# Kernel optimization log

Measured on AMD Instinct MI355X. Metric: run time of the kernel, lower is better.

## Reference

```python
import jax, jax.numpy as jnp
import numpy as np

B, T, E, D, V, L, A = 32, 800, 512, 1024, 5000, 149, 512
SOS, EOS = 1, 2


def setup_inputs() -> dict:
    key = jax.random.key(0)
    ks = jax.random.split(key, 20)
    s = 0.02
    inp = {
        'hpad': jax.random.normal(ks[0], (B, T, E), dtype=jnp.float32),
        'hlen': jax.random.randint(ks[1], (B,), T // 2, T + 1),
        'ys': jax.random.randint(ks[2], (B, L), 3, V),
        # embedding + output projection
        'embed': jax.random.normal(ks[3], (V, D), dtype=jnp.float32) * s,
        'W_out': jax.random.normal(ks[4], (V, D), dtype=jnp.float32) * s,
        'b_out': jnp.zeros((V,), dtype=jnp.float32),
        # additive attention params
        'W_enc': jax.random.normal(ks[5], (E, A), dtype=jnp.float32) * s,
        'W_dec': jax.random.normal(ks[6], (D, A), dtype=jnp.float32) * s,
        'v_att': jax.random.normal(ks[7], (A,), dtype=jnp.float32) * s,
        # LSTMCell layer 0: input = [ey; att_c] of size D+E
        'W_ih0': jax.random.normal(ks[8], (4 * D, D + E), dtype=jnp.float32) * s,
        'b_ih0': jnp.zeros((4 * D,), dtype=jnp.float32),
        'W_hh0': jax.random.normal(ks[9], (4 * D, D), dtype=jnp.float32) * s,
        'b_hh0': jnp.zeros((4 * D,), dtype=jnp.float32),
        # LSTMCell layer 1: input = z0 of size D
        'W_ih1': jax.random.normal(ks[10], (4 * D, D), dtype=jnp.float32) * s,
        'b_ih1': jnp.zeros((4 * D,), dtype=jnp.float32),
        'W_hh1': jax.random.normal(ks[11], (4 * D, D), dtype=jnp.float32) * s,
        'b_hh1': jnp.zeros((4 * D,), dtype=jnp.float32),
    }
    return inp


def _lstm_cell(x, h, c, W_ih, b_ih, W_hh, b_hh):
    # torch.nn.LSTMCell gate order: i, f, g, o
    g = x @ W_ih.T + b_ih + h @ W_hh.T + b_hh
    i, f, gg, o = jnp.split(g, 4, axis=-1)
    c2 = jax.nn.sigmoid(f) * c + jax.nn.sigmoid(i) * jnp.tanh(gg)
    h2 = jax.nn.sigmoid(o) * jnp.tanh(c2)
    return h2, c2


def reference(hpad, hlen, ys, embed, W_out, b_out, W_enc, W_dec, v_att,
              W_ih0, b_ih0, W_hh0, b_hh0, W_ih1, b_ih1, W_hh1, b_hh1):
    mask = jnp.arange(T)[None, :] < hlen[:, None]          # [B,T]
    hpad = hpad * mask[..., None]                          # mask_by_length
    ys_in = jnp.concatenate([jnp.full((B, 1), SOS, ys.dtype), ys], axis=1)   # [B,L+1]
    ys_out = jnp.concatenate([ys, jnp.full((B, 1), EOS, ys.dtype)], axis=1)  # [B,L+1]
    eys = embed[ys_in]                                     # [B,L+1,D]
    pe = jnp.einsum('bte,ea->bta', hpad, W_enc)            # precomputed enc proj

    def step(carry, ey):
        z0, c0, z1, c1 = carry
        # additive attention: e = v^T tanh(W_enc h + W_dec z0)
        e = jnp.einsum('bta,a->bt', jnp.tanh(pe + (z0 @ W_dec)[:, None, :]), v_att)
        e = jnp.where(mask, e, -1e30)
        w = jax.nn.softmax(e, axis=-1)                     # [B,T]
        att_c = jnp.einsum('bt,bte->be', w, hpad)          # [B,E]
        z0, c0 = _lstm_cell(jnp.concatenate([ey, att_c], axis=1), z0, c0,
                            W_ih0, b_ih0, W_hh0, b_hh0)
        z1, c1 = _lstm_cell(z0, z1, c1, W_ih1, b_ih1, W_hh1, b_hh1)
        logits = z1 @ W_out.T + b_out                      # [B,V]
        return (z0, c0, z1, c1), logits

    z = jnp.zeros((B, D), dtype=hpad.dtype)
    carry0 = (z, z, z, z)
    _, logits = jax.lax.scan(step, carry0, eys.transpose(1, 0, 2))  # [L+1,B,V]
    logits = logits.transpose(1, 0, 2)                     # [B,L+1,V]

    logp = jax.nn.log_softmax(logits, axis=-1)
    nll = -jnp.take_along_axis(logp, ys_out[..., None], axis=-1)[..., 0]
    # F.cross_entropy mean, then * (mean(len ys_in) - 1) = * L
    loss = nll.mean() * L
    acc = (jnp.argmax(logits, axis=-1) == ys_out).mean()
    return loss, acc
```

## Files before the change

### kernel.cpp

```cpp
#include <hip/hip_runtime.h>


typedef unsigned short u16;
typedef unsigned char u8;
typedef long long i64;
typedef unsigned long long u64;
typedef float f32x4 __attribute__((ext_vector_type(4)));
typedef float f32x2 __attribute__((ext_vector_type(2)));
typedef short s16x8 __attribute__((ext_vector_type(8)));

constexpr int cB = 32, cT = 800, cE = 512, cD = 1024, cV = 5000, cL = 149,
              cNS = 150, cA = 512;
constexpr int SOS = 1, EOS = 2;
constexpr int NBLK = 256;
constexpr float DS = 1.0f / 128.0f;

__device__ __forceinline__ float bf2f(u16 x){
  union { unsigned u; float f; } v; v.u = ((unsigned)x) << 16; return v.f;
}
__device__ __forceinline__ u16 f2bf(float f){
  union { float f; unsigned u; } v; v.f = f;
  unsigned r = v.u + 0x7FFFu + ((v.u >> 16) & 1u);
  return (u16)(r >> 16);
}
__device__ __forceinline__ float frcp(float x){ return __builtin_amdgcn_rcpf(x); }
__device__ __forceinline__ float fsigm(float x){ return frcp(1.f + __expf(-x)); }
__device__ __forceinline__ float ftanh(float x){
  float u = __expf(2.f * x);
  return 1.f - 2.f * frcp(u + 1.f);
}
__device__ __forceinline__ f32x4 MFMA(s16x8 a, s16x8 b, f32x4 c){
  return __builtin_amdgcn_mfma_f32_16x16x32_bf16(a, b, c, 0, 0, 0);
}
__device__ __forceinline__ f32x4 MFMA8(i64 a, i64 b, f32x4 c){
  return __builtin_amdgcn_mfma_f32_16x16x32_fp8_fp8(a, b, c, 0, 0, 0);
}
__device__ __forceinline__ s16x8 LD8(const u16* p){ return *(const s16x8*)p; }
__device__ __forceinline__ u8 f2fp8(float x){
  return (u8)(__builtin_amdgcn_cvt_pk_fp8_f32(x, x, 0, false) & 0xFF);
}
__device__ __forceinline__ unsigned pk4(float a, float b, float c, float d){
  unsigned w = (unsigned)__builtin_amdgcn_cvt_pk_fp8_f32(a, b, 0, false);
  w = (unsigned)__builtin_amdgcn_cvt_pk_fp8_f32(c, d, (int)w, true);
  return w;
}
__device__ __forceinline__ void unpack8(unsigned lo, unsigned hi, float* o){
  f32x2 a = __builtin_amdgcn_cvt_pk_f32_fp8((int)lo, false);
  f32x2 b = __builtin_amdgcn_cvt_pk_f32_fp8((int)lo, true);
  f32x2 c = __builtin_amdgcn_cvt_pk_f32_fp8((int)hi, false);
  f32x2 d = __builtin_amdgcn_cvt_pk_f32_fp8((int)hi, true);
  o[0]=a[0]; o[1]=a[1]; o[2]=b[0]; o[3]=b[1];
  o[4]=c[0]; o[5]=c[1]; o[6]=d[0]; o[7]=d[1];
}

__device__ __forceinline__ float ld_sc(const float* p){
  return __hip_atomic_load(p, __ATOMIC_RELAXED, __HIP_MEMORY_SCOPE_AGENT);
}
__device__ __forceinline__ void st_sc(float* p, float v){
  __hip_atomic_store(p, v, __ATOMIC_RELAXED, __HIP_MEMORY_SCOPE_AGENT);
}
__device__ __forceinline__ u64 ld_sc8(const void* p){
  return __hip_atomic_load((const u64*)p, __ATOMIC_RELAXED, __HIP_MEMORY_SCOPE_AGENT);
}
__device__ __forceinline__ void st_scb(u8* p, u8 v){
  __hip_atomic_store(p, v, __ATOMIC_RELAXED, __HIP_MEMORY_SCOPE_AGENT);
}

__global__ void k_init(int* bar, float* q, float* c0, float* c1, u8* z1f8,
                       float* att_acc, float* att_l){
  int i = blockIdx.x * blockDim.x + threadIdx.x, n = gridDim.x * blockDim.x;
  for (int k = i; k < 512; k += n) bar[k] = 0;
  for (int k = i; k < cB * cA; k += n) q[k] = 0.f;
  for (int k = i; k < 2 * cB * cD; k += n){ c0[k] = 0.f; c1[k] = 0.f; }
  for (int k = i; k < cB * cD / 4; k += n) ((unsigned*)z1f8)[k] = 0;
  for (int k = i; k < cB * cE; k += n) att_acc[k] = 0.f;
  for (int k = i; k < cB; k += n) att_l[k] = 0.f;
}

__global__ void k_cvt(const float* __restrict__ s, u16* __restrict__ d, int n4){
  int i = blockIdx.x * blockDim.x + threadIdx.x, st = gridDim.x * blockDim.x;
  for (int k = i; k < n4; k += st){
    float4 v = ((const float4*)s)[k];
    ushort4 o; o.x = f2bf(v.x); o.y = f2bf(v.y); o.z = f2bf(v.z); o.w = f2bf(v.w);
    ((ushort4*)d)[k] = o;
  }
}

__global__ void k_cvt8I(const float* __restrict__ s, u8* __restrict__ d, int n){
  int i = blockIdx.x * blockDim.x + threadIdx.x, st = gridDim.x * blockDim.x;
  for (int k = i; k < n; k += st){
    int row = k >> 6, grp = k & 63;
    const float4* p = (const float4*)(s + (size_t)row * 512 + grp * 8);
    float4 v0 = p[0], v1 = p[1];
    unsigned lo = pk4(v0.x, v0.y, v0.z, v0.w);
    unsigned hi = pk4(v1.x, v1.y, v1.z, v1.w);
    *(uint2*)(d + (size_t)row * 1024 + grp * 16 + 8) = make_uint2(lo, hi);
  }
}

__global__ void k_slice(const float* __restrict__ s, u16* __restrict__ d, int n,
                        int cshift, int srcld, int coff){
  int i = blockIdx.x * blockDim.x + threadIdx.x, st = gridDim.x * blockDim.x;
  int cmask = (1 << cshift) - 1;
  for (int k = i; k < n; k += st){
    int r = k >> cshift, c = k & cmask;
    d[k] = f2bf(s[(size_t)r * srcld + coff + c]);
  }
}

__global__ void k_transp(const float* __restrict__ s, u16* __restrict__ d, int n,
                         int rshift, int csrc){
  int i = blockIdx.x * blockDim.x + threadIdx.x, st = gridDim.x * blockDim.x;
  int mask = (1 << rshift) - 1;
  for (int k = i; k < n; k += st){
    int dd = k & mask, a = k >> rshift;
    d[k] = f2bf(s[(size_t)dd * csrc + a]);
  }
}

__global__ void k_bias(const float* a, const float* b, float* o, int n){
  int i = blockIdx.x * blockDim.x + threadIdx.x, st = gridDim.x * blockDim.x;
  for (int k = i; k < n; k += st) o[k] = a[k] + b[k];
}

__global__ void k_wf8perm(const float* __restrict__ s, u8* __restrict__ d,
                          int n4, int kshift, int srcld, int coff){
  int i = blockIdx.x * blockDim.x + threadIdx.x, st = gridDim.x * blockDim.x;
  int kmask = (1 << kshift) - 1;
  for (int k = i; k < n4; k += st){
    int flat = k * 4;
    int R = flat >> kshift, kk = flat & kmask;
    int j = R >> 5, jj = R & 31, g = jj >> 3, c = jj & 7;
    const float* p = s + (size_t)(g * 1024 + j * 8 + c) * srcld + coff + kk;
    ((unsigned*)d)[k] = pk4(p[0]*16.f, p[1]*16.f, p[2]*16.f, p[3]*16.f);
  }
}

__global__ void k_wf8(const float* __restrict__ s, u8* __restrict__ d, int n4){
  int i = blockIdx.x * blockDim.x + threadIdx.x, st = gridDim.x * blockDim.x;
  for (int k = i; k < n4; k += st){
    float4 v = ((const float4*)s)[k];
    ((unsigned*)d)[k] = pk4(v.x*16.f, v.y*16.f, v.z*16.f, v.w*16.f);
  }
}

__global__ void k_wf8t(const float* __restrict__ s, u8* __restrict__ d, int n4){
  int i = blockIdx.x * blockDim.x + threadIdx.x, st = gridDim.x * blockDim.x;
  for (int k = i; k < n4; k += st){
    int flat = k * 4;
    int a = flat >> 10, dd = flat & 1023;
    ((unsigned*)d)[k] = pk4(s[(size_t)(dd+0)*512 + a]*16.f,
                            s[(size_t)(dd+1)*512 + a]*16.f,
                            s[(size_t)(dd+2)*512 + a]*16.f,
                            s[(size_t)(dd+3)*512 + a]*16.f);
  }
}

__global__ void k_gather(const u16* __restrict__ embb, const int* __restrict__ ys,
                         u16* __restrict__ ey, int n16){
  int i = blockIdx.x * blockDim.x + threadIdx.x, st = gridDim.x * blockDim.x;
  for (int k = i; k < n16; k += st){
    int r = k >> 7, seg = k & 127;
    int s = r >> 5, b = r & 31;
    int tok = (s == 0) ? SOS : ys[b * cL + (s - 1)];
    ((uint4*)ey)[(size_t)r * 128 + seg] =
        ((const uint4*)embb)[(size_t)tok * 128 + seg];
  }
}

__global__ __launch_bounds__(512, 1) void k_pe2(const u16* __restrict__ A,
    const u16* __restrict__ Bw, u8* __restrict__ ph8){
  int tid = threadIdx.x, w = tid >> 6, l = tid & 63;
  int col = l & 15, kin = 8 * (l >> 4);
  int mw = w >> 2, nw = w & 3;
  int m0 = blockIdx.x * 128 + mw * 64;
  int n0 = nw * 128;
  f32x4 acc[4][8] = {};
// ... 7 lines not shown
    #pragma unroll
    for (int i = 0; i < 4; ++i)
      #pragma unroll
      for (int j = 0; j < 8; ++j) acc[i][j] = MFMA(af[i], bf[j], acc[i][j]);
  }
  int hi4 = (l >> 4) * 4;
  #pragma unroll
  for (int i = 0; i < 4; ++i)
    #pragma unroll
    for (int j = 0; j < 8; ++j){
      int a0 = n0 + j * 16 + col;
      size_t boff = ((size_t)(a0 >> 3) << 4) + (a0 & 7);
      #pragma unroll
      for (int r = 0; r < 4; ++r){
        int row = m0 + i * 16 + hi4 + r;
        ph8[(size_t)row * 1024 + boff] = f2fp8(acc[i][j][r]);
      }
    }
}

__global__ __launch_bounds__(512, 1) void k_ey2(const u16* __restrict__ ey,
    const u16* __restrict__ Wm, const float* __restrict__ bih0,
    const float* __restrict__ bhh0, u16* __restrict__ eyproj,
    float* __restrict__ g0buf){
  int tid = threadIdx.x, w = tid >> 6, l = tid & 63;
  int col = l & 15, kin = 8 * (l >> 4);
  int mw = w >> 2, nw = w & 3;
  int m0 = blockIdx.x * 128 + mw * 64;
  int n0 = blockIdx.y * 512 + nw * 128;
  f32x4 acc[4][8] = {};
  for (int kc = 0; kc < 32; ++kc){
    int k = kc * 32 + kin;
    s16x8 af[4], bf[8];
    #pragma unroll
    for (int i = 0; i < 4; ++i){
      int ar = m0 + i * 16 + col; ar = (ar < 4800) ? ar : 0;
      af[i] = LD8(ey + (size_t)ar * 1024 + k);
    }
    #pragma unroll
    for (int j = 0; j < 8; ++j) bf[j] = LD8(Wm + (size_t)(n0 + j*16 + col)*1024 + k);
    #pragma unroll
    for (int i = 0; i < 4; ++i)
      #pragma unroll
      for (int j = 0; j < 8; ++j) acc[i][j] = MFMA(af[i], bf[j], acc[i][j]);
  }
  int hi4 = (l >> 4) * 4;
  #pragma unroll
  for (int i = 0; i < 4; ++i)
    #pragma unroll
    for (int j = 0; j < 8; ++j){
      int jc = n0 + j * 16 + col;
      float bj = bih0[jc] + bhh0[jc];
      #pragma unroll
      for (int r = 0; r < 4; ++r){
        int row = m0 + i * 16 + hi4 + r;
        if (row < 4800){
          float val = acc[i][j][r] + bj;
          eyproj[(size_t)row * 4096 + jc] = f2bf(val);
          if (row < 32) g0buf[(size_t)row * 4096 + jc] = val;
        }
      }
    }
}

struct LoopArgs {
  const int* hlen;
  const u8* ph8;
  const u16* eyproj;
  const u8* Wapf8; const u8* Whh1f8; const u8* Wih1f8; const u8* Whh0f8;
  const u8* WdecTf8;
  const float* vatt; const float* bias01;
  float* q; float* att_acc; float* att_l;
  float* g0buf; float* hh1buf; u8* z0f8; u8* z1f8;
  float* c0; float* c1; u16* z1all;
  int* bar;
};

constexpr int SPZ = 1048;
constexpr int SPA = 536;

struct P1Lds { float red[8][512]; float ls[8]; };
struct GvLds { u8 x[32 * SPZ]; float acc[8][2][16][16]; };
union LoopLds { P1Lds p1; GvLds gv; };

__device__ __forceinline__ void gbar(int* bar, int blk, int target){
  __syncthreads();
  if (threadIdx.x == 0){
    asm volatile("s_waitcnt vmcnt(0)" ::: "memory");
    __hip_atomic_store(&bar[blk], target, __ATOMIC_RELAXED, __HIP_MEMORY_SCOPE_AGENT);
  }
  if (blk == NBLK - 1){
    if (threadIdx.x < NBLK){
      while (__hip_atomic_load(&bar[threadIdx.x], __ATOMIC_RELAXED,
                               __HIP_MEMORY_SCOPE_AGENT) < target)
        __builtin_amdgcn_s_sleep(1);
    }
    __syncthreads();
    if (threadIdx.x < 8)
      __hip_atomic_store(&bar[256 + threadIdx.x * 16], target, __ATOMIC_RELAXED,
                         __HIP_MEMORY_SCOPE_AGENT);
  }
  if (threadIdx.x == 0){
    int* rel = &bar[256 + (blk >> 5) * 16];
    while (__hip_atomic_load(rel, __ATOMIC_RELAXED,
                             __HIP_MEMORY_SCOPE_AGENT) < target)
      __builtin_amdgcn_s_sleep(1);
  }
  __syncthreads();
}

__device__ __forceinline__ void stage_att(LoopLds& L, const float* att_acc,
                                          const float* att_l, int tid){
  int r = tid >> 4, c0 = (tid & 15) * 32;
  float sc = 8.0f / ld_sc(att_l + r);
  const float* src = att_acc + r * 512 + c0;
  unsigned wd[8];
  #pragma unroll
  for (int i = 0; i < 8; ++i){
    union { u64 q; float f[2]; } a, b;
    a.q = ld_sc8(src + i * 4);
    b.q = ld_sc8(src + i * 4 + 2);
    wd[i] = pk4(a.f[0] * sc, a.f[1] * sc, b.f[0] * sc, b.f[1] * sc);
  }
  uint2* dst = (uint2*)&L.gv.x[r * SPA + c0];
  dst[0] = make_uint2(wd[0], wd[1]);
  dst[1] = make_uint2(wd[2], wd[3]);
  dst[2] = make_uint2(wd[4], wd[5]);
  dst[3] = make_uint2(wd[6], wd[7]);
}

__device__ __forceinline__ void stage_z(LoopLds& L, const u8* zf8, int tid){
  int r = tid >> 4, c0 = (tid & 15) * 64;
  const u8* src = zf8 + (size_t)r * 1024 + c0;
  u64 v[8];
  #pragma unroll
  for (int i = 0; i < 8; ++i) v[i] = ld_sc8(src + i * 8);
  u64* dst = (u64*)&L.gv.x[r * SPZ + c0];
  #pragma unroll
  for (int i = 0; i < 8; ++i) dst[i] = v[i];
}

template<int KH, int ITERS, int SP>
__device__ __forceinline__ void gemv_reg(const i64* wreg, LoopLds& L, int tid){
  const int w = tid >> 6, l = tid & 63;
  const int col = l & 15, kin = 8 * (l >> 4);
  const int kh = (KH == 4) ? (w & 3) : (w & 1);
  constexpr int KB = ITERS * 32;
  const u8* xr = &L.gv.x[col * SP + kh * KB + kin];
  f32x4 a0 = {0.f,0.f,0.f,0.f}, a1 = {0.f,0.f,0.f,0.f};
  #pragma unroll
  for (int kc = 0; kc < ITERS; ++kc){
    i64 x0 = *(const i64*)(xr + kc * 32);
    i64 x1 = *(const i64*)(xr + 16 * SP + kc * 32);
    a0 = MFMA8(x0, wreg[kc], a0);
    a1 = MFMA8(x1, wreg[kc], a1);
  }
  const int hi4 = (l >> 4) * 4;
  #pragma unroll
  for (int r = 0; r < 4; ++r){
    L.gv.acc[w][0][hi4 + r][col] = a0[r];
    L.gv.acc[w][1][hi4 + r][col] = a1[r];
  }
// ... 30 lines not shown
      const u8* wr2 = g_.Wih1f8 + (size_t)blk * 32 * 1024 +
                      (size_t)(nt4 * 16 + col) * 1024 + kh4 * 256 + kin;
      #pragma unroll
      for (int kc = 0; kc < 8; ++kc) wC[kc] = *(const i64*)(wr2 + kc * 32);
    } else {
      const u8* wr = g_.Whh1f8 + (size_t)(blk - 128) * 32 * 1024 +
                     (size_t)(nt4 * 16 + col) * 1024 + kh4 * 256 + kin;
      #pragma unroll
      for (int kc = 0; kc < 8; ++kc) wB[kc] = *(const i64*)(wr + kc * 32);
      if (blk < 192){
        const u8* wr2 = g_.Whh0f8 + (size_t)(blk - 128) * 64 * 1024 +
                        (size_t)(nt2 * 16 + col) * 1024 + kh2 * 512 + kin;
        #pragma unroll
        for (int kc = 0; kc < 16; ++kc) wC[kc] = *(const i64*)(wr2 + kc * 32);
      } else if (blk < 208){
        const u8* wr2 = g_.WdecTf8 + (size_t)(blk - 192) * 32 * 1024 +
                        (size_t)(nt4 * 16 + col) * 1024 + kh4 * 256 + kin;
        #pragma unroll
        for (int kc = 0; kc < 8; ++kc) wC[kc] = *(const i64*)(wr2 + kc * 32);
      }
    }
  }
  __syncthreads();
  int target = 0;
  for (int s = 0; s < cNS; ++s){
    const int p = s & 1;
    if (nrow > 0){
      float qv[8];
      const float* qb = g_.q + b_att * cA + l * 8;
      #pragma unroll
      for (int i = 0; i < 8; ++i) qv[i] = ld_sc(qb + i);
      float acc8[8] = {0.f,0.f,0.f,0.f,0.f,0.f,0.f,0.f};
      float lsum = 0.f;
      for (int t = t0 + w; t < t1; t += 8){
        uint4 v = *(const uint4*)&ph8_lds[(t - t0) * 1024 + l * 16];
        float x[8]; unpack8(v.x, v.y, x);
        float e_ = 0.f;
        #pragma unroll
        for (int i = 0; i < 8; ++i) e_ += vv[i] * ftanh(x[i] + qv[i]);
        #pragma unroll
        for (int m = 1; m < 64; m <<= 1) e_ += __shfl_xor(e_, m, 64);
        float wt = __expf(e_);
        lsum += wt;
        float h[8]; unpack8(v.z, v.w, h);
        #pragma unroll
        for (int i = 0; i < 8; ++i) acc8[i] = fmaf(wt, h[i], acc8[i]);
      }
      *(f32x4*)&L.p1.red[w][l * 8]     = *(f32x4*)&acc8[0];
      *(f32x4*)&L.p1.red[w][l * 8 + 4] = *(f32x4*)&acc8[4];
      if (l == 0) L.p1.ls[w] = lsum;
      __syncthreads();
      float vsum = 0.f;
      #pragma unroll
      for (int ww = 0; ww < 8; ++ww) vsum += L.p1.red[ww][tid];
      atomicAdd(&g_.att_acc[b_att * cE + tid], vsum);
      if (tid == 0){
        float ls = 0.f;
        #pragma unroll
        for (int i = 0; i < 8; ++i) ls += L.p1.ls[i];
        atomicAdd(&g_.att_l[b_att], ls);
      }
    }
    gbar(g_.bar, blk, ++target);
    if (blk < 128){
      stage_att(L, g_.att_acc, g_.att_l, tid);
      __syncthreads();
      gemv_reg<4, 4, SPA>(wB, L, tid);
      __syncthreads();
      if (tid < 256){
        int b = tid >> 3, dc = tid & 7, d = blk * 8 + dc;
        int mt = b >> 4, rr = b & 15;
        float gate[4];
        #pragma unroll
        for (int g = 0; g < 4; ++g){
          int jj = g * 8 + dc;
          float v = 0.f;
          #pragma unroll
          for (int kh = 0; kh < 4; ++kh)
            v += L.gv.acc[(jj >> 4) * 4 + kh][mt][rr][jj & 15];
          gate[g] = v * DS +
                    ld_sc(&g_.g0buf[(size_t)p * cB * 4096 + b * 4096 + g * 1024 + d]);
        }
        float c = fsigm(gate[1]) * g_.c0[(size_t)p * cB * cD + b * cD + d] +
                  fsigm(gate[0]) * ftanh(gate[2]);
        float z = fsigm(gate[3]) * ftanh(c);
        g_.c0[(size_t)(p ^ 1) * cB * cD + b * cD + d] = c;
        st_scb(&g_.z0f8[b * cD + d], f2fp8(z * 8.f));
      }
    } else {
      stage_z(L, g_.z1f8, tid);
      __syncthreads();
      gemv_reg<4, 8, SPZ>(wB, L, tid);
      __syncthreads();
      const int jb = (blk - 128) * 32;
      #pragma unroll
      for (int it = 0; it < 2; ++it){
        int idx = it * 512 + tid;
        int b = idx >> 5, jj = idx & 31;
        int mt = b >> 4, rr = b & 15;
        float v = 0.f;
        #pragma unroll
        for (int kh = 0; kh < 4; ++kh)
          v += L.gv.acc[(jj >> 4) * 4 + kh][mt][rr][jj & 15];
        st_sc(&g_.hh1buf[b * 4096 + jb + jj], v * DS + g_.bias01[jb + jj]);
      }
    }
    gbar(g_.bar, blk, ++target);
    if (blk < 128){
      stage_z(L, g_.z0f8, tid);
      __syncthreads();
      gemv_reg<4, 8, SPZ>(wC, L, tid);
      __syncthreads();
      if (tid < 256){
        int b = tid >> 3, dc = tid & 7, d = blk * 8 + dc;
        int mt = b >> 4, rr = b & 15;
        float gate[4];
        #pragma unroll
        for (int g = 0; g < 4; ++g){
          int jj = g * 8 + dc;
          float v = 0.f;
          #pragma unroll
          for (int kh = 0; kh < 4; ++kh)
            v += L.gv.acc[(jj >> 4) * 4 + kh][mt][rr][jj & 15];
          gate[g] = v * DS + ld_sc(&g_.hh1buf[b * 4096 + g * 1024 + d]);
        }
        float c = fsigm(gate[1]) * g_.c1[(size_t)p * cB * cD + b * cD + d] +
                  fsigm(gate[0]) * ftanh(gate[2]);
        float z = fsigm(gate[3]) * ftanh(c);
        g_.c1[(size_t)(p ^ 1) * cB * cD + b * cD + d] = c;
        g_.z1all[((size_t)s + 1) * cB * cD + b * cD + d] = f2bf(z);
        st_scb(&g_.z1f8[b * cD + d], f2fp8(z * 8.f));
      }
    } else if (blk < 192){
      stage_z(L, g_.z0f8, tid);
      __syncthreads();
      gemv_reg<2, 16, SPZ>(wC, L, tid);
      __syncthreads();
      if (s < cNS - 1){
        const int jb = (blk - 128) * 64;
        #pragma unroll
        for (int it = 0; it < 4; ++it){
          int idx = it * 512 + tid;
          int b = idx >> 6, jj = idx & 63;
          int mt = b >> 4, rr = b & 15;
          float v = 0.f;
          #pragma unroll
          for (int kh = 0; kh < 2; ++kh)
            v += L.gv.acc[(jj >> 4) * 2 + kh][mt][rr][jj & 15];
          st_sc(&g_.g0buf[(size_t)(p ^ 1) * cB * 4096 + b * 4096 + jb + jj],
                v * DS + bf2f(g_.eyproj[(((size_t)s + 1) * cB + b) * 4096 + jb + jj]));
        }
      }
    } else if (blk < 208){
      stage_z(L, g_.z0f8, tid);
      __syncthreads();
      gemv_reg<4, 8, SPZ>(wC, L, tid);
      __syncthreads();
      if (s < cNS - 1){
        const int jb = (blk - 192) * 32;
        #pragma unroll
        for (int it = 0; it < 2; ++it){
          int idx = it * 512 + tid;
          int b = idx >> 5, jj = idx & 31;
          int mt = b >> 4, rr = b & 15;
          float v = 0.f;
          #pragma unroll
          for (int kh = 0; kh < 4; ++kh)
            v += L.gv.acc[(jj >> 4) * 4 + kh][mt][rr][jj & 15];
          st_sc(&g_.q[b * cA + jb + jj], v * DS);
        }
      }
    } else if (blk == 208){
      for (int i = tid; i < cB * cE; i += 512) st_sc(&g_.att_acc[i], 0.f);
      if (tid < 32) st_sc(&g_.att_l[tid], 0.f);
    }
    gbar(g_.bar, blk, ++target);
  }
}

__global__ __launch_bounds__(256) void k_ce1(const u16* __restrict__ z1all,
    const u16* __restrict__ Woutb, const float* __restrict__ bout,
    const int* __restrict__ ys, float* __restrict__ pmax, float* __restrict__ psum,
    int* __restrict__ pai, float* __restrict__ tgtl){
  int blk = blockIdx.x;
  int sc = blk / 40, vc = blk % 40;
  int tid = threadIdx.x, w = tid >> 6, l = tid & 63;
  int kin = 8 * (l >> 4), col = l & 15;
  int v0 = vc * 128 + w * 32;
  int vA = v0 + col, vB = v0 + 16 + col;
  float boA = (vA < cV) ? bout[vA] : 0.f;
  float boB = (vB < cV) ? bout[vB] : 0.f;
  const u16* wrA = Woutb + (size_t)((vA < cV) ? vA : cV - 1) * cD;
  const u16* wrB = Woutb + (size_t)((vB < cV) ? vB : cV - 1) * cD;
  __shared__ int tgt_sh[32];
  __shared__ float rsm[4][32], rss[4][32];
  __shared__ int rsi[4][32];
  for (int si = 0; si < 5; ++si){
    int s = sc * 5 + si;
    if (tid < 32) tgt_sh[tid] = (s < cL) ? ys[tid * cL + s] : EOS;
// ... 109 lines not shown
  const int*   hlen = (const int*)d_in[1];
  const int*   ys   = (const int*)d_in[2];
  const float* embed= (const float*)d_in[3];
  const float* Wout = (const float*)d_in[4];
  const float* bout = (const float*)d_in[5];
  const float* Wenc = (const float*)d_in[6];
  const float* Wdec = (const float*)d_in[7];
  const float* vatt = (const float*)d_in[8];
  const float* Wih0 = (const float*)d_in[9];
  const float* bih0 = (const float*)d_in[10];
  const float* Whh0 = (const float*)d_in[11];
  const float* bhh0 = (const float*)d_in[12];
  const float* Wih1 = (const float*)d_in[13];
  const float* bih1 = (const float*)d_in[14];
  const float* Whh1 = (const float*)d_in[15];
  const float* bhh1 = (const float*)d_in[16];
  (void)in_sizes; (void)n_in; (void)out_size; (void)ws_size;

  char* base = (char*)d_ws;
  size_t off = 0;
  auto alloc = [&](size_t bytes) -> void* {
    void* r = base + off; off += (bytes + 255) & ~(size_t)255; return r;
  };
  int*   bar     = (int*)  alloc(512 * sizeof(int));
  u16*   hpadM   = (u16*)  alloc((size_t)cB * cT * cE * 2);
  u8*    ph8     = (u8*)   alloc((size_t)cB * cT * 1024);
  u16*   embb    = (u16*)  alloc((size_t)cV * cD * 2);
  u16*   ey      = (u16*)  alloc((size_t)cNS * cB * cD * 2);
  u16*   eyproj  = (u16*)  alloc((size_t)cNS * cB * 4096 * 2);
  u16*   z1all   = (u16*)  alloc((size_t)(cNS + 1) * cB * cD * 2);
  u16*   WencT   = (u16*)  alloc((size_t)cA * cE * 2);
  u16*   Wih0m   = (u16*)  alloc((size_t)4096 * cD * 2);
  u16*   Woutb   = (u16*)  alloc((size_t)cV * cD * 2);
  u8*    Wapf8   = (u8*)   alloc((size_t)4096 * 512);
  u8*    Wih1f8  = (u8*)   alloc((size_t)4096 * 1024);
  u8*    Whh1f8  = (u8*)   alloc((size_t)4096 * 1024);
  u8*    Whh0f8  = (u8*)   alloc((size_t)4096 * 1024);
  u8*    WdecTf8 = (u8*)   alloc((size_t)512 * 1024);
  float* bias01  = (float*)alloc(4096 * 4);
  float* qbuf    = (float*)alloc((size_t)cB * cA * 4);
  float* att_acc = (float*)alloc((size_t)cB * cE * 4);
  float* att_l   = (float*)alloc((size_t)cB * 4);
  float* g0buf   = (float*)alloc((size_t)2 * cB * 4096 * 4);
  float* hh1buf  = (float*)alloc((size_t)cB * 4096 * 4);
  u8*    z0f8    = (u8*)   alloc((size_t)cB * cD);
  u8*    z1f8    = (u8*)   alloc((size_t)cB * cD);
  float* c0      = (float*)alloc((size_t)2 * cB * cD * 4);
  float* c1      = (float*)alloc((size_t)2 * cB * cD * 4);
  float* pmax    = (float*)alloc((size_t)cNS * cB * 40 * 4);
  float* psum    = (float*)alloc((size_t)cNS * cB * 40 * 4);
  int*   pai     = (int*)  alloc((size_t)cNS * cB * 40 * 4);
  float* tgtl    = (float*)alloc((size_t)cNS * cB * 4);
  float* cestep  = (float*)alloc((size_t)cNS * 2 * 4);

  k_init<<<64, 256, 0, stream>>>(bar, qbuf, c0, c1, z1f8, att_acc, att_l);
  k_cvt<<<2048, 256, 0, stream>>>(hpad, hpadM, cB * cT * cE / 4);
  k_cvt8I<<<1024, 256, 0, stream>>>(hpad, ph8, cB * cT * 64);
  k_cvt<<<2048, 256, 0, stream>>>(embed, embb, cV * cD / 4);
  k_cvt<<<2048, 256, 0, stream>>>(Wout, Woutb, cV * cD / 4);
  k_slice<<<1024, 256, 0, stream>>>(Wih0, Wih0m, 4096 * cD, 10, 1536, 0);
  k_transp<<<256, 256, 0, stream>>>(Wenc, WencT, cA * cE, 9, cA);
  k_bias<<<16, 256, 0, stream>>>(bih1, bhh1, bias01, 4096);
  k_wf8perm<<<512, 256, 0, stream>>>(Wih0, Wapf8, 4096 * 512 / 4, 9, 1536, 1024);
  k_wf8perm<<<1024, 256, 0, stream>>>(Wih1, Wih1f8, 4096 * 1024 / 4, 10, 1024, 0);
  k_wf8<<<1024, 256, 0, stream>>>(Whh1, Whh1f8, 4096 * 1024 / 4);
  k_wf8<<<1024, 256, 0, stream>>>(Whh0, Whh0f8, 4096 * 1024 / 4);
  k_wf8t<<<128, 256, 0, stream>>>(Wdec, WdecTf8, 512 * 1024 / 4);
  k_gather<<<1200, 256, 0, stream>>>(embb, ys, ey, cNS * cB * 128);
  k_pe2<<<200, 512, 0, stream>>>(hpadM, WencT, ph8);
  k_ey2<<<dim3(38, 8), 512, 0, stream>>>(ey, Wih0m, bih0, bhh0, eyproj, g0buf);

  LoopArgs la;
  la.hlen = hlen; la.ph8 = ph8; la.eyproj = eyproj;
  la.Wapf8 = Wapf8; la.Whh1f8 = Whh1f8; la.Wih1f8 = Wih1f8;
  la.Whh0f8 = Whh0f8; la.WdecTf8 = WdecTf8;
  la.vatt = vatt; la.bias01 = bias01;
  la.q = qbuf; la.att_acc = att_acc; la.att_l = att_l;
  la.g0buf = g0buf; la.hh1buf = hh1buf; la.z0f8 = z0f8; la.z1f8 = z1f8;
  la.c0 = c0; la.c1 = c1; la.z1all = z1all; la.bar = bar;
  k_loop<<<NBLK, 512, 0, stream>>>(la);

  k_ce1<<<1200, 256, 0, stream>>>(z1all, Woutb, bout, ys, pmax, psum, pai, tgtl);
  k_ce2<<<cNS, 64, 0, stream>>>(pmax, psum, pai, tgtl, ys, cestep);
  k_ce3<<<1, 256, 0, stream>>>(cestep, (float*)d_out);
}
```

Baseline: 4.657 ms.

## Replace grid barriers with step-tagged dataflow flags in persistent decoder loop

```diff
diff --git a/kernel.cpp b/kernel.cpp
--- a/kernel.cpp
+++ b/kernel.cpp
@@ -3,6 +3,7 @@
 
 typedef unsigned short u16;
 typedef unsigned char u8;
+typedef unsigned int u32;
 typedef long long i64;
 typedef unsigned long long u64;
 typedef float f32x4 __attribute__((ext_vector_type(4)));
@@ -16,11 +17,11 @@
 constexpr float DS = 1.0f / 128.0f;
 
 __device__ __forceinline__ float bf2f(u16 x){
-  union { unsigned u; float f; } v; v.u = ((unsigned)x) << 16; return v.f;
+  union { u32 u; float f; } v; v.u = ((u32)x) << 16; return v.f;
 }
 __device__ __forceinline__ u16 f2bf(float f){
-  union { float f; unsigned u; } v; v.f = f;
-  unsigned r = v.u + 0x7FFFu + ((v.u >> 16) & 1u);
+  union { float f; u32 u; } v; v.f = f;
+  u32 r = v.u + 0x7FFFu + ((v.u >> 16) & 1u);
   return (u16)(r >> 16);
 }
 __device__ __forceinline__ float frcp(float x){ return __builtin_amdgcn_rcpf(x); }
@@ -39,12 +40,12 @@
 __device__ __forceinline__ u8 f2fp8(float x){
   return (u8)(__builtin_amdgcn_cvt_pk_fp8_f32(x, x, 0, false) & 0xFF);
 }
-__device__ __forceinline__ unsigned pk4(float a, float b, float c, float d){
-  unsigned w = (unsigned)__builtin_amdgcn_cvt_pk_fp8_f32(a, b, 0, false);
-  w = (unsigned)__builtin_amdgcn_cvt_pk_fp8_f32(c, d, (int)w, true);
+__device__ __forceinline__ u32 pk4(float a, float b, float c, float d){
+  u32 w = (u32)__builtin_amdgcn_cvt_pk_fp8_f32(a, b, 0, false);
+  w = (u32)__builtin_amdgcn_cvt_pk_fp8_f32(c, d, (int)w, true);
   return w;
 }
-__device__ __forceinline__ void unpack8(unsigned lo, unsigned hi, float* o){
+__device__ __forceinline__ void unpack8(u32 lo, u32 hi, float* o){
   f32x2 a = __builtin_amdgcn_cvt_pk_f32_fp8((int)lo, false);
   f32x2 b = __builtin_amdgcn_cvt_pk_f32_fp8((int)lo, true);
   f32x2 c = __builtin_amdgcn_cvt_pk_f32_fp8((int)hi, false);
@@ -62,19 +63,28 @@
 __device__ __forceinline__ u64 ld_sc8(const void* p){
   return __hip_atomic_load((const u64*)p, __ATOMIC_RELAXED, __HIP_MEMORY_SCOPE_AGENT);
 }
-__device__ __forceinline__ void st_scb(u8* p, u8 v){
+__device__ __forceinline__ void st_sc8(void* p, u64 v){
+  __hip_atomic_store((u64*)p, v, __ATOMIC_RELAXED, __HIP_MEMORY_SCOPE_AGENT);
+}
+__device__ __forceinline__ u32 ld_su(const u32* p){
+  return __hip_atomic_load(p, __ATOMIC_RELAXED, __HIP_MEMORY_SCOPE_AGENT);
+}
+__device__ __forceinline__ void st_su(u32* p, u32 v){
   __hip_atomic_store(p, v, __ATOMIC_RELAXED, __HIP_MEMORY_SCOPE_AGENT);
 }
-
-__global__ void k_init(int* bar, float* q, float* c0, float* c1, u8* z1f8,
+__device__ __forceinline__ void st_s16(u16* p, u32 v){
+  asm volatile("global_store_short %0, %1, off sc0 sc1" :: "v"(p), "v"(v) : "memory");
+}
+
+__global__ void k_init(u32* ctl, u32* qt, float* c0, float* c1, u16* z1t,
                        float* att_acc, float* att_l){
   int i = blockIdx.x * blockDim.x + threadIdx.x, n = gridDim.x * blockDim.x;
-  for (int k = i; k < 512; k += n) bar[k] = 0;
-  for (int k = i; k < cB * cA; k += n) q[k] = 0.f;
+  for (int k = i; k < 64; k += n) ctl[k] = 0;
+  for (int k = i; k < cB * cA; k += n) qt[k] = 0;
   for (int k = i; k < 2 * cB * cD; k += n){ c0[k] = 0.f; c1[k] = 0.f; }
-  for (int k = i; k < cB * cD / 4; k += n) ((unsigned*)z1f8)[k] = 0;
-  for (int k = i; k < cB * cE; k += n) att_acc[k] = 0.f;
-  for (int k = i; k < cB; k += n) att_l[k] = 0.f;
+  for (int k = i; k < cB * cD / 2; k += n) ((u32*)z1t)[k] = 0;
+  for (int k = i; k < 2 * cB * cE; k += n) att_acc[k] = 0.f;
+  for (int k = i; k < 2 * cB; k += n) att_l[k] = 0.f;
 }
 
 __global__ void k_cvt(const float* __restrict__ s, u16* __restrict__ d, int n4){
@@ -92,8 +102,8 @@
     int row = k >> 6, grp = k & 63;
     const float4* p = (const float4*)(s + (size_t)row * 512 + grp * 8);
     float4 v0 = p[0], v1 = p[1];
-    unsigned lo = pk4(v0.x, v0.y, v0.z, v0.w);
-    unsigned hi = pk4(v1.x, v1.y, v1.z, v1.w);
+    u32 lo = pk4(v0.x, v0.y, v0.z, v0.w);
+    u32 hi = pk4(v1.x, v1.y, v1.z, v1.w);
     *(uint2*)(d + (size_t)row * 1024 + grp * 16 + 8) = make_uint2(lo, hi);
   }
 }
@@ -132,7 +142,7 @@
     int R = flat >> kshift, kk = flat & kmask;
     int j = R >> 5, jj = R & 31, g = jj >> 3, c = jj & 7;
     const float* p = s + (size_t)(g * 1024 + j * 8 + c) * srcld + coff + kk;
-    ((unsigned*)d)[k] = pk4(p[0]*16.f, p[1]*16.f, p[2]*16.f, p[3]*16.f);
+    ((u32*)d)[k] = pk4(p[0]*16.f, p[1]*16.f, p[2]*16.f, p[3]*16.f);
   }
 }
 
@@ -140,7 +150,7 @@
   int i = blockIdx.x * blockDim.x + threadIdx.x, st = gridDim.x * blockDim.x;
   for (int k = i; k < n4; k += st){
     float4 v = ((const float4*)s)[k];
-    ((unsigned*)d)[k] = pk4(v.x*16.f, v.y*16.f, v.z*16.f, v.w*16.f);
+    ((u32*)d)[k] = pk4(v.x*16.f, v.y*16.f, v.z*16.f, v.w*16.f);
   }
 }
 
@@ -149,10 +159,10 @@
   for (int k = i; k < n4; k += st){
     int flat = k * 4;
     int a = flat >> 10, dd = flat & 1023;
-    ((unsigned*)d)[k] = pk4(s[(size_t)(dd+0)*512 + a]*16.f,
-                            s[(size_t)(dd+1)*512 + a]*16.f,
-                            s[(size_t)(dd+2)*512 + a]*16.f,
-                            s[(size_t)(dd+3)*512 + a]*16.f);
+    ((u32*)d)[k] = pk4(s[(size_t)(dd+0)*512 + a]*16.f,
+                       s[(size_t)(dd+1)*512 + a]*16.f,
+                       s[(size_t)(dd+2)*512 + a]*16.f,
+                       s[(size_t)(dd+3)*512 + a]*16.f);
   }
 }
 
@@ -206,7 +216,7 @@
 __global__ __launch_bounds__(512, 1) void k_ey2(const u16* __restrict__ ey,
     const u16* __restrict__ Wm, const float* __restrict__ bih0,
     const float* __restrict__ bhh0, u16* __restrict__ eyproj,
-    float* __restrict__ g0buf){
+    u32* __restrict__ g0t){
   int tid = threadIdx.x, w = tid >> 6, l = tid & 63;
   int col = l & 15, kin = 8 * (l >> 4);
   int mw = w >> 2, nw = w & 3;
@@ -241,7 +251,7 @@
         if (row < 4800){
           float val = acc[i][j][r] + bj;
           eyproj[(size_t)row * 4096 + jc] = f2bf(val);
-          if (row < 32) g0buf[(size_t)row * 4096 + jc] = val;
+          if (row < 32) g0t[(size_t)row * 4096 + jc] = (u32)f2bf(val);
         }
       }
     }
@@ -254,74 +264,43 @@
   const u8* Wapf8; const u8* Whh1f8; const u8* Wih1f8; const u8* Whh0f8;
   const u8* WdecTf8;
   const float* vatt; const float* bias01;
-  float* q; float* att_acc; float* att_l;
-  float* g0buf; float* hh1buf; u8* z0f8; u8* z1f8;
+  u32* qt; float* att_acc; float* att_l;
+  u32* g0t; u32* hh1t; u16* z0t; u16* z1t;
   float* c0; float* c1; u16* z1all;
-  int* bar;
+  u32* ctl;
 };
 
 constexpr int SPZ = 1048;
 constexpr int SPA = 536;
 
 struct P1Lds { float red[8][512]; float ls[8]; };
-struct GvLds { u8 x[32 * SPZ]; float acc[8][2][16][16]; };
+struct GvLds { u8 x[32 * SPZ]; float acc[8][2][16][17]; };
 union LoopLds { P1Lds p1; GvLds gv; };
 
-__device__ __forceinline__ void gbar(int* bar, int blk, int target){
-  __syncthreads();
-  if (threadIdx.x == 0){
-    asm volatile("s_waitcnt vmcnt(0)" ::: "memory");
-    __hip_atomic_store(&bar[blk], target, __ATOMIC_RELAXED, __HIP_MEMORY_SCOPE_AGENT);
-  }
-  if (blk == NBLK - 1){
-    if (threadIdx.x < NBLK){
-      while (__hip_atomic_load(&bar[threadIdx.x], __ATOMIC_RELAXED,
-                               __HIP_MEMORY_SCOPE_AGENT) < target)
-        __builtin_amdgcn_s_sleep(1);
-    }
-    __syncthreads();
-    if (threadIdx.x < 8)
-      __hip_atomic_store(&bar[256 + threadIdx.x * 16], target, __ATOMIC_RELAXED,
-                         __HIP_MEMORY_SCOPE_AGENT);
-  }
-  if (threadIdx.x == 0){
-    int* rel = &bar[256 + (blk >> 5) * 16];
-    while (__hip_atomic_load(rel, __ATOMIC_RELAXED,
-                             __HIP_MEMORY_SCOPE_AGENT) < target)
-      __builtin_amdgcn_s_sleep(1);
-  }
-  __syncthreads();
-}
-
-__device__ __forceinline__ void stage_att(LoopLds& L, const float* att_acc,
-                                          const float* att_l, int tid){
-  int r = tid >> 4, c0 = (tid & 15) * 32;
-  float sc = 8.0f / ld_sc(att_l + r);
-  const float* src = att_acc + r * 512 + c0;
-  unsigned wd[8];
+template<int SP>
+__device__ __forceinline__ void stage_ztag(LoopLds& L, const u16* zt, int tid,
+                                           int tag){
+  int r = tid >> 4, cb = (tid & 15) * 64;
+  const u16* src = zt + (size_t)r * 1024 + cb;
+  const u64 tmask = 0xFF00FF00FF00FF00ULL;
+  const u64 texp = 0x0100010001000100ULL * (u64)(tag & 0xFF);
+  u64 v[16];
+  for(;;){
+    bool ok = true;
+    #pragma unroll
+    for (int i = 0; i < 16; ++i) v[i] = ld_sc8(src + i * 4);
+    #pragma unroll
+    for (int i = 0; i < 16; ++i) ok &= ((v[i] & tmask) == texp);
+    if (__all(ok)) break;
+    __builtin_amdgcn_s_sleep(1);
+  }
+  u64* dst = (u64*)&L.gv.x[r * SP + cb];
   #pragma unroll
   for (int i = 0; i < 8; ++i){
-    union { u64 q; float f[2]; } a, b;
-    a.q = ld_sc8(src + i * 4);
-    b.q = ld_sc8(src + i * 4 + 2);
-    wd[i] = pk4(a.f[0] * sc, a.f[1] * sc, b.f[0] * sc, b.f[1] * sc);
-  }
-  uint2* dst = (uint2*)&L.gv.x[r * SPA + c0];
-  dst[0] = make_uint2(wd[0], wd[1]);
-  dst[1] = make_uint2(wd[2], wd[3]);
-  dst[2] = make_uint2(wd[4], wd[5]);
-  dst[3] = make_uint2(wd[6], wd[7]);
-}
-
-__device__ __forceinline__ void stage_z(LoopLds& L, const u8* zf8, int tid){
-  int r = tid >> 4, c0 = (tid & 15) * 64;
-  const u8* src = zf8 + (size_t)r * 1024 + c0;
-  u64 v[8];
-  #pragma unroll
-  for (int i = 0; i < 8; ++i) v[i] = ld_sc8(src + i * 8);
-  u64* dst = (u64*)&L.gv.x[r * SPZ + c0];
-  #pragma unroll
-  for (int i = 0; i < 8; ++i) dst[i] = v[i];
+    u32 lo = __builtin_amdgcn_perm((u32)(v[2*i] >> 32),   (u32)v[2*i],   0x06040200u);
+    u32 hi = __builtin_amdgcn_perm((u32)(v[2*i+1] >> 32), (u32)v[2*i+1], 0x06040200u);
+    dst[i] = ((u64)hi << 32) | lo;
+  }
 }
 
 template<int KH, int ITERS, int SP>
@@ -398,54 +377,136 @@
     }
   }
   __syncthreads();
-  int target = 0;
+
   for (int s = 0; s < cNS; ++s){
     const int p = s & 1;
-    if (nrow > 0){
-      float qv[8];
-      const float* qb = g_.q + b_att * cA + l * 8;
-      #pragma unroll
-      for (int i = 0; i < 8; ++i) qv[i] = ld_sc(qb + i);
-      float acc8[8] = {0.f,0.f,0.f,0.f,0.f,0.f,0.f,0.f};
-      float lsum = 0.f;
-      for (int t = t0 + w; t < t1; t += 8){
-        uint4 v = *(const uint4*)&ph8_lds[(t - t0) * 1024 + l * 16];
-        float x[8]; unpack8(v.x, v.y, x);
-        float e_ = 0.f;
-        #pragma unroll
-        for (int i = 0; i < 8; ++i) e_ += vv[i] * ftanh(x[i] + qv[i]);
-        #pragma unroll
-        for (int m = 1; m < 64; m <<= 1) e_ += __shfl_xor(e_, m, 64);
-        float wt = __expf(e_);
-        lsum += wt;
-        float h[8]; unpack8(v.z, v.w, h);
-        #pragma unroll
-        for (int i = 0; i < 8; ++i) acc8[i] = fmaf(wt, h[i], acc8[i]);
-      }
-      *(f32x4*)&L.p1.red[w][l * 8]     = *(f32x4*)&acc8[0];
-      *(f32x4*)&L.p1.red[w][l * 8 + 4] = *(f32x4*)&acc8[4];
-      if (l == 0) L.p1.ls[w] = lsum;
-      __syncthreads();
-      float vsum = 0.f;
-      #pragma unroll
-      for (int ww = 0; ww < 8; ++ww) vsum += L.p1.red[ww][tid];
-      atomicAdd(&g_.att_acc[b_att * cE + tid], vsum);
+    u64 eyw = 0;
+    {
+      const u32* qrow = g_.qt + b_att * cA + l * 8;
+      u64 qw[4];
+      const u64 tmaskq = 0xFFFF0000FFFF0000ULL;
+      const u64 texpq  = ((u64)(u32)s << 16) | ((u64)(u32)s << 48);
+      for(;;){
+        bool ok = true;
+        #pragma unroll
+        for (int i = 0; i < 4; ++i){
+          qw[i] = ld_sc8(qrow + i * 2);
+          ok &= ((qw[i] & tmaskq) == texpq);
+        }
+        if (__all(ok)) break;
+        __builtin_amdgcn_s_sleep(1);
+      }
+      if (nrow > 0){
+        float qv[8];
+        #pragma unroll
+        for (int i = 0; i < 4; ++i){
+          qv[2*i]   = bf2f((u16)(qw[i] & 0xFFFF));
+          qv[2*i+1] = bf2f((u16)((qw[i] >> 32) & 0xFFFF));
+        }
+        float acc8[8] = {0.f,0.f,0.f,0.f,0.f,0.f,0.f,0.f};
+        float lsum = 0.f;
+        for (int t = t0 + w; t < t1; t += 8){
+          uint4 v = *(const uint4*)&ph8_lds[(t - t0) * 1024 + l * 16];
+          float x[8]; unpack8(v.x, v.y, x);
+          float e_ = 0.f;
+          #pragma unroll
+          for (int i = 0; i < 8; ++i) e_ += vv[i] * ftanh(x[i] + qv[i]);
+          #pragma unroll
+          for (int m = 1; m < 64; m <<= 1) e_ += __shfl_xor(e_, m, 64);
+          float wt = __expf(e_);
+          lsum += wt;
+          float h[8]; unpack8(v.z, v.w, h);
+          #pragma unroll
+          for (int i = 0; i < 8; ++i) acc8[i] = fmaf(wt, h[i], acc8[i]);
+        }
+        *(f32x4*)&L.p1.red[w][l * 8]     = *(f32x4*)&acc8[0];
+        *(f32x4*)&L.p1.red[w][l * 8 + 4] = *(f32x4*)&acc8[4];
+        if (l == 0) L.p1.ls[w] = lsum;
+        __syncthreads();
+        float vsum = 0.f;
+        #pragma unroll
+        for (int ww = 0; ww < 8; ++ww) vsum += L.p1.red[ww][tid];
+        if (tid == 0){
+          while (ld_su(&g_.ctl[48 + 8*p]) < (u32)(s >> 1))
+            __builtin_amdgcn_s_sleep(2);
+        }
+        __syncthreads();
+        atomicAdd(&g_.att_acc[((size_t)p*cB + b_att)*cE + tid], vsum);
+        if (tid == 0){
+          float ls = 0.f;
+          #pragma unroll
+          for (int i = 0; i < 8; ++i) ls += L.p1.ls[i];
+          atomicAdd(&g_.att_l[p*cB + b_att], ls);
+        }
+      }
+      __syncthreads();
+      if (tid == 0)
+        __hip_atomic_fetch_add(&g_.ctl[b_att], 1u, __ATOMIC_RELAXED,
+                               __HIP_MEMORY_SCOPE_AGENT);
+    }
+    if (blk < 128){
       if (tid == 0){
-        float ls = 0.f;
-        #pragma unroll
-        for (int i = 0; i < 8; ++i) ls += L.p1.ls[i];
-        atomicAdd(&g_.att_l[b_att], ls);
-      }
-    }
-    gbar(g_.bar, blk, ++target);
-    if (blk < 128){
-      stage_att(L, g_.att_acc, g_.att_l, tid);
-      __syncthreads();
+        u32 tgt = 8u * (u32)(s + 1);
+        for(;;){
+          bool ok = true;
+          #pragma unroll
+          for (int i = 0; i < 16; ++i){
+            u64 v = ld_sc8(&g_.ctl[i * 2]);
+            ok &= ((u32)v >= tgt) && ((u32)(v >> 32) >= tgt);
+          }
+          if (ok) break;
+          __builtin_amdgcn_s_sleep(2);
+        }
+      }
+      __syncthreads();
+      {
+        int r = tid >> 4, cc = (tid & 15) * 32;
+        const float* src = g_.att_acc + ((size_t)p*cB + r)*cE + cc;
+        float lsm = ld_sc(g_.att_l + p*cB + r);
+        u64 av[16];
+        #pragma unroll
+        for (int i = 0; i < 16; ++i) av[i] = ld_sc8(src + i*2);
+        float sc = 8.0f / lsm;
+        u32 wd[8];
+        #pragma unroll
+        for (int j = 0; j < 8; ++j){
+          union { u64 q; float f[2]; } a, b;
+          a.q = av[2*j]; b.q = av[2*j+1];
+          wd[j] = pk4(a.f[0]*sc, a.f[1]*sc, b.f[0]*sc, b.f[1]*sc);
+        }
+        u64* dst = (u64*)&L.gv.x[r * SPA + cc];
+        #pragma unroll
+        for (int j = 0; j < 4; ++j) dst[j] = ((u64)wd[2*j+1] << 32) | wd[2*j];
+      }
+      __syncthreads();
+      if (tid == 0)
+        __hip_atomic_fetch_add(&g_.ctl[32 + 8*p], 1u, __ATOMIC_RELAXED,
+                               __HIP_MEMORY_SCOPE_AGENT);
+      u32 gw[4]; bool gok = true;
+      int bb = tid >> 3, dc = tid & 7, d = blk * 8 + dc;
+      if (tid < 256){
+        #pragma unroll
+        for (int g = 0; g < 4; ++g){
+          gw[g] = ld_su(&g_.g0t[(size_t)bb*4096 + g*1024 + d]);
+          gok &= ((gw[g] >> 16) == (u32)s);
+        }
+      }
       gemv_reg<4, 4, SPA>(wB, L, tid);
       __syncthreads();
       if (tid < 256){
-        int b = tid >> 3, dc = tid & 7, d = blk * 8 + dc;
-        int mt = b >> 4, rr = b & 15;
+        if (!__all(gok)){
+          for(;;){
+            bool ok = true;
+            #pragma unroll
+            for (int g = 0; g < 4; ++g){
+              gw[g] = ld_su(&g_.g0t[(size_t)bb*4096 + g*1024 + d]);
+              ok &= ((gw[g] >> 16) == (u32)s);
+            }
+            if (__all(ok)) break;
+            __builtin_amdgcn_s_sleep(1);
+          }
+        }
+        int mt = bb >> 4, rr = bb & 15;
         float gate[4];
         #pragma unroll
         for (int g = 0; g < 4; ++g){
@@ -454,42 +515,70 @@
           #pragma unroll
           for (int kh = 0; kh < 4; ++kh)
             v += L.gv.acc[(jj >> 4) * 4 + kh][mt][rr][jj & 15];
-          gate[g] = v * DS +
-                    ld_sc(&g_.g0buf[(size_t)p * cB * 4096 + b * 4096 + g * 1024 + d]);
-        }
-        float c = fsigm(gate[1]) * g_.c0[(size_t)p * cB * cD + b * cD + d] +
+          gate[g] = v * DS + bf2f((u16)(gw[g] & 0xFFFF));
+        }
+        float c = fsigm(gate[1]) * g_.c0[(size_t)p*cB*cD + bb*cD + d] +
                   fsigm(gate[0]) * ftanh(gate[2]);
         float z = fsigm(gate[3]) * ftanh(c);
-        g_.c0[(size_t)(p ^ 1) * cB * cD + b * cD + d] = c;
-        st_scb(&g_.z0f8[b * cD + d], f2fp8(z * 8.f));
+        g_.c0[(size_t)(p ^ 1)*cB*cD + bb*cD + d] = c;
+        st_s16(&g_.z0t[bb * cD + d],
+               (u32)(f2fp8(z * 8.f) | (((s + 1) & 0xFF) << 8)));
       }
     } else {
-      stage_z(L, g_.z1f8, tid);
+      if (blk < 192 && s < cNS - 1){
+        int b = tid >> 4, j4 = (tid & 15) * 4;
+        eyw = *(const u64*)(g_.eyproj + (((size_t)(s+1)*cB + b)*4096) +
+                            (blk - 128) * 64 + j4);
+      }
+      stage_ztag<SPZ>(L, g_.z1t, tid, s);
       __syncthreads();
       gemv_reg<4, 8, SPZ>(wB, L, tid);
       __syncthreads();
-      const int jb = (blk - 128) * 32;
-      #pragma unroll
-      for (int it = 0; it < 2; ++it){
-        int idx = it * 512 + tid;
-        int b = idx >> 5, jj = idx & 31;
+      {
+        const int jb = (blk - 128) * 32;
+        int b = tid >> 4, j2 = (tid & 15) * 2;
         int mt = b >> 4, rr = b & 15;
-        float v = 0.f;
-        #pragma unroll
-        for (int kh = 0; kh < 4; ++kh)
-          v += L.gv.acc[(jj >> 4) * 4 + kh][mt][rr][jj & 15];
-        st_sc(&g_.hh1buf[b * 4096 + jb + jj], v * DS + g_.bias01[jb + jj]);
-      }
-    }
-    gbar(g_.bar, blk, ++target);
+        u32 ow[2];
+        #pragma unroll
+        for (int k = 0; k < 2; ++k){
+          int jj = j2 + k;
+          float v = 0.f;
+          #pragma unroll
+          for (int kh = 0; kh < 4; ++kh)
+            v += L.gv.acc[(jj >> 4)*4 + kh][mt][rr][jj & 15];
+          ow[k] = ((u32)(s + 1) << 16) | f2bf(v * DS + g_.bias01[jb + jj]);
+        }
+        st_sc8(&g_.hh1t[(size_t)b*4096 + jb + j2], ((u64)ow[1] << 32) | ow[0]);
+      }
+    }
     if (blk < 128){
-      stage_z(L, g_.z0f8, tid);
-      __syncthreads();
+      stage_ztag<SPZ>(L, g_.z0t, tid, s + 1);
+      __syncthreads();
+      u32 hw[4]; bool hok = true;
+      int bb = tid >> 3, dc = tid & 7, d = blk * 8 + dc;
+      if (tid < 256){
+        #pragma unroll
+        for (int g = 0; g < 4; ++g){
+          hw[g] = ld_su(&g_.hh1t[(size_t)bb*4096 + g*1024 + d]);
+          hok &= ((hw[g] >> 16) == (u32)(s + 1));
+        }
+      }
       gemv_reg<4, 8, SPZ>(wC, L, tid);
       __syncthreads();
       if (tid < 256){
-        int b = tid >> 3, dc = tid & 7, d = blk * 8 + dc;
-        int mt = b >> 4, rr = b & 15;
+        if (!__all(hok)){
+          for(;;){
+            bool ok = true;
+            #pragma unroll
+            for (int g = 0; g < 4; ++g){
+              hw[g] = ld_su(&g_.hh1t[(size_t)bb*4096 + g*1024 + d]);
+              ok &= ((hw[g] >> 16) == (u32)(s + 1));
+            }
+            if (__all(ok)) break;
+            __builtin_amdgcn_s_sleep(1);
+          }
+        }
+        int mt = bb >> 4, rr = bb & 15;
         float gate[4];
         #pragma unroll
         for (int g = 0; g < 4; ++g){
@@ -498,59 +587,74 @@
           #pragma unroll
           for (int kh = 0; kh < 4; ++kh)
             v += L.gv.acc[(jj >> 4) * 4 + kh][mt][rr][jj & 15];
-          gate[g] = v * DS + ld_sc(&g_.hh1buf[b * 4096 + g * 1024 + d]);
-        }
-        float c = fsigm(gate[1]) * g_.c1[(size_t)p * cB * cD + b * cD + d] +
+          gate[g] = v * DS + bf2f((u16)(hw[g] & 0xFFFF));
+        }
+        float c = fsigm(gate[1]) * g_.c1[(size_t)p*cB*cD + bb*cD + d] +
                   fsigm(gate[0]) * ftanh(gate[2]);
         float z = fsigm(gate[3]) * ftanh(c);
-        g_.c1[(size_t)(p ^ 1) * cB * cD + b * cD + d] = c;
-        g_.z1all[((size_t)s + 1) * cB * cD + b * cD + d] = f2bf(z);
-        st_scb(&g_.z1f8[b * cD + d], f2fp8(z * 8.f));
+        g_.c1[(size_t)(p ^ 1)*cB*cD + bb*cD + d] = c;
+        g_.z1all[((size_t)s + 1)*cB*cD + bb*cD + d] = f2bf(z);
+        st_s16(&g_.z1t[bb * cD + d],
+               (u32)(f2fp8(z * 8.f) | (((s + 1) & 0xFF) << 8)));
       }
     } else if (blk < 192){
-      stage_z(L, g_.z0f8, tid);
+      stage_ztag<SPZ>(L, g_.z0t, tid, s + 1);
       __syncthreads();
       gemv_reg<2, 16, SPZ>(wC, L, tid);
       __syncthreads();
       if (s < cNS - 1){
         const int jb = (blk - 128) * 64;
-        #pragma unroll
-        for (int it = 0; it < 4; ++it){
-          int idx = it * 512 + tid;
-          int b = idx >> 6, jj = idx & 63;
-          int mt = b >> 4, rr = b & 15;
+        int b = tid >> 4, j4 = (tid & 15) * 4;
+        int mt = b >> 4, rr = b & 15;
+        u32 ow[4];
+        #pragma unroll
+        for (int k = 0; k < 4; ++k){
+          int jj = j4 + k;
           float v = 0.f;
           #pragma unroll
           for (int kh = 0; kh < 2; ++kh)
-            v += L.gv.acc[(jj >> 4) * 2 + kh][mt][rr][jj & 15];
-          st_sc(&g_.g0buf[(size_t)(p ^ 1) * cB * 4096 + b * 4096 + jb + jj],
-                v * DS + bf2f(g_.eyproj[(((size_t)s + 1) * cB + b) * 4096 + jb + jj]));
-        }
+            v += L.gv.acc[(jj >> 4)*2 + kh][mt][rr][jj & 15];
+          ow[k] = ((u32)(s + 1) << 16) |
+                  f2bf(v * DS + bf2f(((const u16*)&eyw)[k]));
+        }
+        st_sc8(&g_.g0t[(size_t)b*4096 + jb + j4],     ((u64)ow[1] << 32) | ow[0]);
+        st_sc8(&g_.g0t[(size_t)b*4096 + jb + j4 + 2], ((u64)ow[3] << 32) | ow[2]);
       }
     } else if (blk < 208){
-      stage_z(L, g_.z0f8, tid);
+      stage_ztag<SPZ>(L, g_.z0t, tid, s + 1);
       __syncthreads();
       gemv_reg<4, 8, SPZ>(wC, L, tid);
       __syncthreads();
       if (s < cNS - 1){
         const int jb = (blk - 192) * 32;
-        #pragma unroll
-        for (int it = 0; it < 2; ++it){
-          int idx = it * 512 + tid;
-          int b = idx >> 5, jj = idx & 31;
-          int mt = b >> 4, rr = b & 15;
+        int b = tid >> 4, j2 = (tid & 15) * 2;
+        int mt = b >> 4, rr = b & 15;
+        u32 ow[2];
+        #pragma unroll
+        for (int k = 0; k < 2; ++k){
+          int jj = j2 + k;
           float v = 0.f;
           #pragma unroll
           for (int kh = 0; kh < 4; ++kh)
-            v += L.gv.acc[(jj >> 4) * 4 + kh][mt][rr][jj & 15];
-          st_sc(&g_.q[b * cA + jb + jj], v * DS);
-        }
+            v += L.gv.acc[(jj >> 4)*4 + kh][mt][rr][jj & 15];
+          ow[k] = ((u32)(s + 1) << 16) | f2bf(v * DS);
+        }
+        st_sc8(&g_.qt[(size_t)b*cA + jb + j2], ((u64)ow[1] << 32) | ow[0]);
       }
     } else if (blk == 208){
-      for (int i = tid; i < cB * cE; i += 512) st_sc(&g_.att_acc[i], 0.f);
-      if (tid < 32) st_sc(&g_.att_l[tid], 0.f);
-    }
-    gbar(g_.bar, blk, ++target);
+      if (tid == 0){
+        u32 tgt = 128u * ((u32)(s >> 1) + 1u);
+        while (ld_su(&g_.ctl[32 + 8*p]) < tgt) __builtin_amdgcn_s_sleep(4);
+      }
+      __syncthreads();
+      {
+        float* aa = g_.att_acc + (size_t)p*cB*cE;
+        for (int i = tid; i < cB*cE; i += 512) st_sc(&aa[i], 0.f);
+        if (tid < cB) st_sc(&g_.att_l[p*cB + tid], 0.f);
+      }
+      __syncthreads();
+      if (tid == 0) st_su(&g_.ctl[48 + 8*p], (u32)(s >> 1) + 1u);
+    }
   }
 }
 
@@ -706,7 +810,7 @@
   auto alloc = [&](size_t bytes) -> void* {
     void* r = base + off; off += (bytes + 255) & ~(size_t)255; return r;
   };
-  int*   bar     = (int*)  alloc(512 * sizeof(int));
+  u32*   ctl     = (u32*)  alloc(1024);
   u16*   hpadM   = (u16*)  alloc((size_t)cB * cT * cE * 2);
   u8*    ph8     = (u8*)   alloc((size_t)cB * cT * 1024);
   u16*   embb    = (u16*)  alloc((size_t)cV * cD * 2);
@@ -722,13 +826,13 @@
   u8*    Whh0f8  = (u8*)   alloc((size_t)4096 * 1024);
   u8*    WdecTf8 = (u8*)   alloc((size_t)512 * 1024);
   float* bias01  = (float*)alloc(4096 * 4);
-  float* qbuf    = (float*)alloc((size_t)cB * cA * 4);
-  float* att_acc = (float*)alloc((size_t)cB * cE * 4);
-  float* att_l   = (float*)alloc((size_t)cB * 4);
-  float* g0buf   = (float*)alloc((size_t)2 * cB * 4096 * 4);
-  float* hh1buf  = (float*)alloc((size_t)cB * 4096 * 4);
-  u8*    z0f8    = (u8*)   alloc((size_t)cB * cD);
-  u8*    z1f8    = (u8*)   alloc((size_t)cB * cD);
+  u32*   qt      = (u32*)  alloc((size_t)cB * cA * 4);
+  float* att_acc = (float*)alloc((size_t)2 * cB * cE * 4);
+  float* att_l   = (float*)alloc((size_t)2 * cB * 4);
+  u32*   g0t     = (u32*)  alloc((size_t)cB * 4096 * 4);
+  u32*   hh1t    = (u32*)  alloc((size_t)cB * 4096 * 4);
+  u16*   z0t     = (u16*)  alloc((size_t)cB * cD * 2);
+  u16*   z1t     = (u16*)  alloc((size_t)cB * cD * 2);
   float* c0      = (float*)alloc((size_t)2 * cB * cD * 4);
   float* c1      = (float*)alloc((size_t)2 * cB * cD * 4);
   float* pmax    = (float*)alloc((size_t)cNS * cB * 40 * 4);
@@ -737,7 +841,7 @@
   float* tgtl    = (float*)alloc((size_t)cNS * cB * 4);
   float* cestep  = (float*)alloc((size_t)cNS * 2 * 4);
 
-  k_init<<<64, 256, 0, stream>>>(bar, qbuf, c0, c1, z1f8, att_acc, att_l);
+  k_init<<<64, 256, 0, stream>>>(ctl, qt, c0, c1, z1t, att_acc, att_l);
   k_cvt<<<2048, 256, 0, stream>>>(hpad, hpadM, cB * cT * cE / 4);
   k_cvt8I<<<1024, 256, 0, stream>>>(hpad, ph8, cB * cT * 64);
   k_cvt<<<2048, 256, 0, stream>>>(embed, embb, cV * cD / 4);
@@ -752,16 +856,16 @@
   k_wf8t<<<128, 256, 0, stream>>>(Wdec, WdecTf8, 512 * 1024 / 4);
   k_gather<<<1200, 256, 0, stream>>>(embb, ys, ey, cNS * cB * 128);
   k_pe2<<<200, 512, 0, stream>>>(hpadM, WencT, ph8);
-  k_ey2<<<dim3(38, 8), 512, 0, stream>>>(ey, Wih0m, bih0, bhh0, eyproj, g0buf);
+  k_ey2<<<dim3(38, 8), 512, 0, stream>>>(ey, Wih0m, bih0, bhh0, eyproj, g0t);
 
   LoopArgs la;
   la.hlen = hlen; la.ph8 = ph8; la.eyproj = eyproj;
   la.Wapf8 = Wapf8; la.Whh1f8 = Whh1f8; la.Wih1f8 = Wih1f8;
   la.Whh0f8 = Whh0f8; la.WdecTf8 = WdecTf8;
   la.vatt = vatt; la.bias01 = bias01;
-  la.q = qbuf; la.att_acc = att_acc; la.att_l = att_l;
-  la.g0buf = g0buf; la.hh1buf = hh1buf; la.z0f8 = z0f8; la.z1f8 = z1f8;
-  la.c0 = c0; la.c1 = c1; la.z1all = z1all; la.bar = bar;
+  la.qt = qt; la.att_acc = att_acc; la.att_l = att_l;
+  la.g0t = g0t; la.hh1t = hh1t; la.z0t = z0t; la.z1t = z1t;
+  la.c0 = c0; la.c1 = c1; la.z1all = z1all; la.ctl = ctl;
   k_loop<<<NBLK, 512, 0, stream>>>(la);
 
   k_ce1<<<1200, 256, 0, stream>>>(z1all, Woutb, bout, ys, pmax, psum, pai, tgtl);
```

After: 8.061 ms. 73.1% more time.
